# Performance work log

Hardware: AMD Instinct MI355X
Metric: run time of the kernel (lower is better)

Reference implementation:

```python
import jax, jax.numpy as jnp
import numpy as np

N_NODES = 100000
N_EDGES = 1600000
IN_CH = 256
OUT_CH = 64
BN_EPS = 1e-5


def gcn_conv(x, edge_index, W, b, n_nodes):
    # PyG GCNConv: h = x @ W; add self-loops; symmetric normalization; scatter-add at dst; + bias
    h = x @ W  # [N, out]
    loop = jnp.arange(n_nodes, dtype=edge_index.dtype)
    src = jnp.concatenate([edge_index[0], loop])
    dst = jnp.concatenate([edge_index[1], loop])
    deg = jnp.zeros((n_nodes,), h.dtype).at[dst].add(jnp.ones((), h.dtype))
    dinv = jnp.where(deg > 0, jax.lax.rsqrt(deg), 0.0)
    norm = dinv[src] * dinv[dst]  # [E+N]
    msg = h[src] * norm[:, None]  # gather + scale
    out = jax.ops.segment_sum(msg, dst, num_segments=n_nodes)
    return out + b


def batch_norm(x, gamma, beta):
    mu = x.mean(axis=0)
    var = x.var(axis=0)  # biased, as torch BN training stats
    return (x - mu) * jax.lax.rsqrt(var + BN_EPS) * gamma + beta


def setup_inputs() -> dict:
    key = jax.random.key(0)
    ks = jax.random.split(key, 8)
    x = jax.random.normal(ks[0], (N_NODES, IN_CH), dtype=jnp.float32)
    edge_index = jax.random.randint(ks[1], (2, N_EDGES), 0, N_NODES, dtype=jnp.int32)
    def glorot(k, fan_in, fan_out):
        s = (6.0 / (fan_in + fan_out)) ** 0.5
        return jax.random.uniform(k, (fan_in, fan_out), jnp.float32, -s, s)
    return {
        "x": x,
        "edge_index": edge_index,
        "W1": glorot(ks[2], IN_CH, 128), "b1": jnp.zeros((128,), jnp.float32),
        "gamma1": jnp.ones((128,), jnp.float32), "beta1": jnp.zeros((128,), jnp.float32),
        "W2": glorot(ks[3], 128, 64), "b2": jnp.zeros((64,), jnp.float32),
        "gamma2": jnp.ones((64,), jnp.float32), "beta2": jnp.zeros((64,), jnp.float32),
        "W3": glorot(ks[4], 64, OUT_CH), "b3": jnp.zeros((OUT_CH,), jnp.float32),
    }


def reference(x, edge_index, W1, b1, gamma1, beta1, W2, b2, gamma2, beta2, W3, b3):
    n = x.shape[0]
    h = gcn_conv(x, edge_index, W1, b1, n)
    h = jax.nn.relu(batch_norm(h, gamma1, beta1))  # dropout = identity (eval)
    h = gcn_conv(h, edge_index, W2, b2, n)
    h = jax.nn.relu(batch_norm(h, gamma2, beta2))
    z = gcn_conv(h, edge_index, W3, b3, n)
    return z
```

## Files before the change

### kernel.cpp

```cpp
#include <hip/hip_runtime.h>
#include <cstdint>
#include <cstddef>

#define IN_CH 256

constexpr float BN_EPS = 1e-5f;

using u16x4 = __attribute__((ext_vector_type(4))) unsigned short;
using u16x8 = __attribute__((ext_vector_type(8))) unsigned short;
using bf16x8 = __attribute__((ext_vector_type(8))) short;
using f32x4 = __attribute__((ext_vector_type(4))) float;

__device__ __forceinline__ unsigned short f2bf_rne(float x) {
  unsigned u = __builtin_bit_cast(unsigned, x);
  unsigned r = u + 0x7FFFu + ((u >> 16) & 1u);
  return (unsigned short)(r >> 16);
}
__device__ __forceinline__ float bf2f(unsigned short h) {
  unsigned u = ((unsigned)h) << 16;
  return __builtin_bit_cast(float, u);
}


#define NBK_MAX 400

__global__ __launch_bounds__(256) void bucket_hist(const int* __restrict__ dst,
                                                   int* __restrict__ bcnt, int E, int nbk) {
  __shared__ int c[NBK_MAX];
  for (int j = threadIdx.x; j < nbk; j += 256) c[j] = 0;
  __syncthreads();
  for (int i = blockIdx.x * 256 + threadIdx.x; i < E; i += gridDim.x * 256)
    atomicAdd(&c[dst[i] >> 8], 1);
  __syncthreads();
  for (int j = threadIdx.x; j < nbk; j += 256)
    if (c[j]) atomicAdd(&bcnt[j], c[j]);
}

__global__ void bucket_scan(const int* __restrict__ bcnt, int* __restrict__ boff,
                            int* __restrict__ gcur, int E, int nbk) {
  __shared__ int lds[512];
  int t = threadIdx.x;
  int v = (t < nbk) ? bcnt[t] : 0;
  lds[t] = v;
  __syncthreads();
  for (int s = 1; s < 512; s <<= 1) {
    int x = (t >= s) ? lds[t - s] : 0;
    __syncthreads();
    lds[t] += x;
    __syncthreads();
  }
  if (t < nbk) {
    boff[t] = lds[t] - v;
    gcur[t] = lds[t] - v;
  }
  if (t == 0) boff[nbk] = E;
}

__global__ __launch_bounds__(256) void partition(const int* __restrict__ src,
                                                 const int* __restrict__ dst,
                                                 int* __restrict__ gcur,
                                                 unsigned* __restrict__ part, int E, int nbk) {
  __shared__ int cnt[NBK_MAX];
  __shared__ int base[NBK_MAX];
  const int t = threadIdx.x;
  for (int j = t; j < nbk; j += 256) cnt[j] = 0;
  __syncthreads();
  const int e0 = blockIdx.x * 4096;
  unsigned mypk[16];
  int mybk[16];
#pragma unroll
  for (int u = 0; u < 16; ++u) {
    int e = e0 + u * 256 + t;
    if (e < E) {
      int d = dst[e];
      mypk[u] = (unsigned)src[e] | ((unsigned)(d & 255) << 17);
      mybk[u] = d >> 8;
      atomicAdd(&cnt[mybk[u]], 1);
    } else {
      mybk[u] = -1;
    }
  }
  __syncthreads();
  for (int j = t; j < nbk; j += 256) {
    int c = cnt[j];
    base[j] = c ? atomicAdd(&gcur[j], c) : 0;
    cnt[j] = 0;
  }
  __syncthreads();
#pragma unroll
  for (int u = 0; u < 16; ++u) {
    if (mybk[u] >= 0) {
      int r = atomicAdd(&cnt[mybk[u]], 1);
      part[base[mybk[u]] + r] = mypk[u];
    }
  }
}

__global__ __launch_bounds__(256) void bucket_csr(const unsigned* __restrict__ part,
                                                  const int* __restrict__ boff,
                                                  int* __restrict__ offs, int* __restrict__ srcs,
                                                  float* __restrict__ dinv, int N, int E) {
  __shared__ unsigned pk[8192];
  __shared__ int ssrc[8192];
  __shared__ int cnt[256];
  __shared__ int offl[256];
  __shared__ int cur[256];
  const int b = blockIdx.x;
  const int t = threadIdx.x;
  const int e0 = boff[b];
  int ne = boff[b + 1] - e0;
  if (ne > 8192) ne = 8192;
  cnt[t] = 0;
  __syncthreads();
  for (int i = t; i < ne; i += 256) {
    unsigned v = part[e0 + i];
    pk[i] = v;
    atomicAdd(&cnt[v >> 17], 1);
  }
  __syncthreads();
  int vv = cnt[t];
  offl[t] = vv;
  __syncthreads();
  for (int s = 1; s < 256; s <<= 1) {
    int x = (t >= s) ? offl[t - s] : 0;
    __syncthreads();
    offl[t] += x;
    __syncthreads();
  }
  int excl = offl[t] - vv;
  cur[t] = excl;
  __syncthreads();
  for (int i = t; i < ne; i += 256) {
    unsigned p = pk[i];
    int dl = p >> 17;
    int r = atomicAdd(&cur[dl], 1);
    ssrc[r] = (int)(p & 0x1FFFF);
  }
  __syncthreads();
  for (int i = t; i < ne; i += 256) srcs[e0 + i] = ssrc[i];
  int node = b * 256 + t;
  if (node < N) {
    offs[node] = e0 + excl;
    dinv[node] = rsqrtf((float)(vv + 1));
  }
  if (b == gridDim.x - 1 && t == 0) offs[N] = E;
}


__global__ void wprep(const float* __restrict__ W, unsigned short* __restrict__ hi,
                      unsigned short* __restrict__ lo, int K, int N) {
  int i = blockIdx.x * 256 + threadIdx.x;
  if (i >= K * N) return;
  int k = i / N, n = i - k * N;
  float v = W[i];
  unsigned short h = f2bf_rne(v);
  hi[(size_t)n * K + k] = h;
  lo[(size_t)n * K + k] = f2bf_rne(v - bf2f(h));
}


template <int K, int BN, int SLICES, bool BNRELU>
__global__ __launch_bounds__(256) void mfma_gemm(const float* __restrict__ A,
                                                 const unsigned short* __restrict__ Bt_hi,
                                                 const unsigned short* __restrict__ Bt_lo,
                                                 const float* __restrict__ ss,
                                                 const float* __restrict__ dinv,
                                                 unsigned short* __restrict__ Out, int M) {
  constexpr int BM = 128;
  constexpr int CS = BN / SLICES;
  __shared__ unsigned short Ah[BM * 32];
  __shared__ unsigned short Al[BM * 32];
  __shared__ unsigned short Bh[BN * 32];
  __shared__ unsigned short Bl[BN * 32];

  const int tid = threadIdx.x;
  const int wave = tid >> 6;
  const int lane = tid & 63;
  const int lg = lane >> 4;
  const int lr = lane & 15;
  const int row0 = blockIdx.x * BM;

  f32x4 acc[2][BN / 16];
#pragma unroll
  for (int f = 0; f < 2; ++f)
#pragma unroll
    for (int j = 0; j < BN / 16; ++j) acc[f][j] = (f32x4){0.f, 0.f, 0.f, 0.f};

  for (int k0 = 0; k0 < K; k0 += 32) {
    __syncthreads();
#pragma unroll
    for (int it = 0; it < 4; ++it) {
      int m = it * 32 + (tid >> 3);
      int c2 = tid & 7;
      float4 v = {0.f, 0.f, 0.f, 0.f};
      if (row0 + m < M) v = *(const float4*)&A[(size_t)(row0 + m) * K + k0 + c2 * 4];
      if constexpr (BNRELU) {
        int kk = k0 + c2 * 4;
        float4 sc = *(const float4*)&ss[kk];
        float4 sh = *(const float4*)&ss[K + kk];
        v.x = fmaxf(0.f, fmaf(v.x, sc.x, sh.x));
        v.y = fmaxf(0.f, fmaf(v.y, sc.y, sh.y));
        v.z = fmaxf(0.f, fmaf(v.z, sc.z, sh.z));
        v.w = fmaxf(0.f, fmaf(v.w, sc.w, sh.w));
      }
      float vv[4] = {v.x, v.y, v.z, v.w};
      u16x4 h4, l4;
#pragma unroll
      for (int i = 0; i < 4; ++i) {
        unsigned short h = f2bf_rne(vv[i]);
        h4[i] = h;
        l4[i] = f2bf_rne(vv[i] - bf2f(h));
      }
      int pr = (m >> 1) & 3;
      int base = m * 32 + (((c2 >> 1) ^ pr) * 8) + (c2 & 1) * 4;
      *(u16x4*)&Ah[base] = h4;
      *(u16x4*)&Al[base] = l4;
    }
#pragma unroll
    for (int it = 0; it < BN / 64; ++it) {
      int n = it * 64 + (tid >> 2);
      int c = tid & 3;
      int pr = (n >> 1) & 3;
      int base = n * 32 + ((c ^ pr) * 8);
      *(u16x8*)&Bh[base] = *(const u16x8*)&Bt_hi[(size_t)n * K + k0 + c * 8];
      *(u16x8*)&Bl[base] = *(const u16x8*)&Bt_lo[(size_t)n * K + k0 + c * 8];
    }
    __syncthreads();

    bf16x8 afh[2], afl[2];
#pragma unroll
    for (int f = 0; f < 2; ++f) {
      int m = wave * 32 + f * 16 + lr;
      int pr = (m >> 1) & 3;
      int base = m * 32 + ((lg ^ pr) * 8);
      afh[f] = *(const bf16x8*)&Ah[base];
      afl[f] = *(const bf16x8*)&Al[base];
    }
#pragma unroll
    for (int j = 0; j < BN / 16; ++j) {
      int n = j * 16 + lr;
      int pr = (n >> 1) & 3;
      int base = n * 32 + ((lg ^ pr) * 8);
      bf16x8 bh = *(const bf16x8*)&Bh[base];
      bf16x8 bl = *(const bf16x8*)&Bl[base];
#pragma unroll
      for (int f = 0; f < 2; ++f) {
        acc[f][j] = __builtin_amdgcn_mfma_f32_16x16x32_bf16(afh[f], bh, acc[f][j], 0, 0, 0);
        acc[f][j] = __builtin_amdgcn_mfma_f32_16x16x32_bf16(afl[f], bh, acc[f][j], 0, 0, 0);
        acc[f][j] = __builtin_amdgcn_mfma_f32_16x16x32_bf16(afh[f], bl, acc[f][j], 0, 0, 0);
      }
    }
  }

#pragma unroll
  for (int f = 0; f < 2; ++f) {
#pragma unroll
    for (int r4 = 0; r4 < 4; ++r4) {
      int r = row0 + wave * 32 + f * 16 + lg * 4 + r4;
      if (r >= M) continue;
      float dv = dinv[r];
#pragma unroll
      for (int j = 0; j < BN / 16; ++j) {
        int c = j * 16 + lr;
        int slice = c / CS;
        int wi = c % CS;
        Out[((size_t)slice * M + r) * CS + wi] = f2bf_rne(acc[f][j][r4] * dv);
      }
    }
  }
}


template <int C, int NSLICE, bool STATS, bool BIAS>
__global__ __launch_bounds__(256) void agg_slice(const unsigned short* __restrict__ g,
                                                 const int* __restrict__ offs,
                                                 const int* __restrict__ srcs,
                                                 const float* __restrict__ dinv,
                                                 const float* __restrict__ bias,
                                                 float* __restrict__ out,
                                                 float* __restrict__ stat, int N) {
  constexpr int CS = C / NSLICE;
  constexpr int LPE = CS / 2;
  constexpr int NPW = 64 / LPE;
  constexpr int T = 128 / (4 * NPW);
  const int s = blockIdx.x;
  const int w = threadIdx.x >> 6;
  const int lane = threadIdx.x & 63;
  const int gi = lane / LPE;
  const int ch2 = lane % LPE;
  const unsigned short* gs = g + (size_t)s * N * CS;
  const size_t cb = (size_t)ch2 * 2;

  float sx = 0.f, sy = 0.f, qx = 0.f, qy = 0.f;

#pragma unroll
  for (int it = 0; it < T; ++it) {
    int node = blockIdx.y * 128 + it * (4 * NPW) + w * NPW + gi;
    if (node < N) {
      unsigned u = *(const unsigned*)&gs[(size_t)node * CS + cb];
      float ax = __builtin_bit_cast(float, u << 16);
      float ay = __builtin_bit_cast(float, u & 0xffff0000u);

      const int e0 = offs[node], e1 = offs[node + 1];
      const int nb = (e1 - e0 + 7) >> 3;
      int sA[8], sB[8];
#pragma unroll
      for (int j = 0; j < 8; ++j) sA[j] = srcs[e0 + j];
      for (int b = 0; b < nb; ++b) {
        const int base = e0 + b * 8;
#pragma unroll
        for (int j = 0; j < 8; ++j) sB[j] = srcs[base + 8 + j];
        unsigned uu[8];
#pragma unroll
        for (int j = 0; j < 8; ++j) {
          uu[j] = 0u;
          if (base + j < e1) uu[j] = *(const unsigned*)&gs[(size_t)sA[j] * CS + cb];
        }
#pragma unroll
        for (int j = 0; j < 8; ++j) {
          ax += __builtin_bit_cast(float, uu[j] << 16);
          ay += __builtin_bit_cast(float, uu[j] & 0xffff0000u);
        }
#pragma unroll
        for (int j = 0; j < 8; ++j) sA[j] = sB[j];
      }
      float dv = dinv[node];
      float ox = ax * dv, oy = ay * dv;
      if constexpr (BIAS) {
        ox += bias[s * CS + cb];
        oy += bias[s * CS + cb + 1];
      }
      *(float2*)&out[(size_t)node * C + s * CS + cb] = (float2){ox, oy};
      if constexpr (STATS) {
        sx += ox;
        sy += oy;
        qx += ox * ox;
        qy += oy * oy;
      }
    }
  }

  if constexpr (STATS) {
    __shared__ float red[256][4];
    red[threadIdx.x][0] = sx;
    red[threadIdx.x][1] = sy;
    red[threadIdx.x][2] = qx;
    red[threadIdx.x][3] = qy;
    __syncthreads();
    if (threadIdx.x < LPE) {
      float a0 = 0.f, a1 = 0.f, a2 = 0.f, a3 = 0.f;
      for (int k = threadIdx.x; k < 256; k += LPE) {
        a0 += red[k][0];
        a1 += red[k][1];
        a2 += red[k][2];
        a3 += red[k][3];
      }
      atomicAdd(&stat[s * CS + threadIdx.x * 2], a0);
      atomicAdd(&stat[s * CS + threadIdx.x * 2 + 1], a1);
      atomicAdd(&stat[C + s * CS + threadIdx.x * 2], a2);
      atomicAdd(&stat[C + s * CS + threadIdx.x * 2 + 1], a3);
    }
  }
}


template <int C>
__global__ void bn_finalize(const float* __restrict__ stat, const float* __restrict__ gamma,
                            const float* __restrict__ beta, float* __restrict__ ss, int N) {
  int c = threadIdx.x;
  if (c >= C) return;
  float mu = stat[c] / (float)N;
  float var = stat[C + c] / (float)N - mu * mu;
  float rs = rsqrtf(var + BN_EPS);
  float sc = gamma[c] * rs;
  ss[c] = sc;
  ss[C + c] = beta[c] - mu * sc;
}


extern "C" void kernel_launch(void* const* d_in, const int* in_sizes, int n_in, void* d_out,
                              int out_size, void* d_ws, size_t ws_size, hipStream_t stream) {
  const float* x = (const float*)d_in[0];
  const int* ei = (const int*)d_in[1];
  const float* W1 = (const float*)d_in[2];
  const float* gamma1 = (const float*)d_in[4];
  const float* beta1 = (const float*)d_in[5];
  const float* W2 = (const float*)d_in[6];
  const float* gamma2 = (const float*)d_in[8];
  const float* beta2 = (const float*)d_in[9];
  const float* W3 = (const float*)d_in[10];
  const float* b3 = (const float*)d_in[11];
  float* out = (float*)d_out;

  const int N = in_sizes[0] / IN_CH;
  const int E = in_sizes[1] / 2;
  const int* e_src = ei;
  const int* e_dst = ei + E;
  const int nbk = (N + 255) >> 8;

  char* ws = (char*)d_ws;
  size_t off = 0;
  auto alloc = [&](size_t bytes) {
    size_t r = off;
    off += (bytes + 1023) & ~(size_t)1023;
    return r;
  };
  int* bcnt = (int*)(ws + alloc(NBK_MAX * 4));
  int* boff = (int*)(ws + alloc((NBK_MAX + 1) * 4));
  int* gcur = (int*)(ws + alloc(NBK_MAX * 4));
  unsigned* part = (unsigned*)(ws + alloc((size_t)E * 4));
  int* offs = (int*)(ws + alloc((size_t)(N + 1) * 4));
  int* srcs = (int*)(ws + alloc(((size_t)E + 32) * 4));
  float* dinv = (float*)(ws + alloc((size_t)N * 4));
  unsigned short* Wt1h = (unsigned short*)(ws + alloc(256 * 128 * 2));
  unsigned short* Wt1l = (unsigned short*)(ws + alloc(256 * 128 * 2));
  unsigned short* Wt2h = (unsigned short*)(ws + alloc(128 * 64 * 2));
  unsigned short* Wt2l = (unsigned short*)(ws + alloc(128 * 64 * 2));
  unsigned short* Wt3h = (unsigned short*)(ws + alloc(64 * 64 * 2));
  unsigned short* Wt3l = (unsigned short*)(ws + alloc(64 * 64 * 2));
  float* stat1 = (float*)(ws + alloc(256 * 4));
  float* stat2 = (float*)(ws + alloc(128 * 4));
  float* ss1 = (float*)(ws + alloc(256 * 4));
  float* ss2 = (float*)(ws + alloc(128 * 4));
  unsigned short* g = (unsigned short*)(ws + alloc((size_t)N * 128 * 2));
  float* h = (float*)(ws + alloc((size_t)N * 128 * 4));

  hipMemsetAsync(bcnt, 0, NBK_MAX * 4, stream);
  hipMemsetAsync(stat1, 0, 256 * 4, stream);
  hipMemsetAsync(stat2, 0, 128 * 4, stream);

  bucket_hist<<<2048, 256, 0, stream>>>(e_dst, bcnt, E, nbk);
  bucket_scan<<<1, 512, 0, stream>>>(bcnt, boff, gcur, E, nbk);
  partition<<<(E + 4095) / 4096, 256, 0, stream>>>(e_src, e_dst, gcur, part, E, nbk);
  bucket_csr<<<nbk, 256, 0, stream>>>(part, boff, offs, srcs, dinv, N, E);

  wprep<<<(256 * 128 + 255) / 256, 256, 0, stream>>>(W1, Wt1h, Wt1l, 256, 128);
  wprep<<<(128 * 64 + 255) / 256, 256, 0, stream>>>(W2, Wt2h, Wt2l, 128, 64);
  wprep<<<(64 * 64 + 255) / 256, 256, 0, stream>>>(W3, Wt3h, Wt3l, 64, 64);

  const int gM = (N + 127) / 128;
  const int nch = (N + 127) / 128;
  const dim3 gAgg1(8, nch);
  const dim3 gAgg2(4, nch);

  mfma_gemm<256, 128, 8, false><<<gM, 256, 0, stream>>>(x, Wt1h, Wt1l, nullptr, dinv, g, N);
  agg_slice<128, 8, true, false><<<gAgg1, 256, 0, stream>>>(g, offs, srcs, dinv, nullptr, h,
                                                            stat1, N);
  bn_finalize<128><<<1, 128, 0, stream>>>(stat1, gamma1, beta1, ss1, N);

  mfma_gemm<128, 64, 4, true><<<gM, 256, 0, stream>>>(h, Wt2h, Wt2l, ss1, dinv, g, N);
  agg_slice<64, 4, true, false><<<gAgg2, 256, 0, stream>>>(g, offs, srcs, dinv, nullptr, h,
                                                           stat2, N);
  bn_finalize<64><<<1, 64, 0, stream>>>(stat2, gamma2, beta2, ss2, N);

  mfma_gemm<64, 64, 4, true><<<gM, 256, 0, stream>>>(h, Wt3h, Wt3l, ss2, dinv, g, N);
  agg_slice<64, 4, false, true><<<gAgg2, 256, 0, stream>>>(g, offs, srcs, dinv, b3, out, nullptr,
                                                           N);
}
```

Measured before the change: 371.9 us.

## Store intermediate activations as bf16 and widen aggregation lanes to 4 channels

Intermediate aggregated features between layers are now written as bf16 instead of fp32, and the following GEMM reads bf16 directly. This halves the write and read traffic on the hidden buffer. The aggregation kernel now has each lane own 4 channels (8-byte gathers) rather than 2, with source indices pre-shifted into byte offsets to save address arithmetic. It also uses nontemporal loads and stores for the index stream and outputs. The risk is extra rounding in the intermediate activations, and fewer lanes per edge could change gather efficiency.

```diff
diff --git a/kernel.cpp b/kernel.cpp
--- a/kernel.cpp
+++ b/kernel.cpp
@@ -19,6 +19,12 @@
 __device__ __forceinline__ float bf2f(unsigned short h) {
   unsigned u = ((unsigned)h) << 16;
   return __builtin_bit_cast(float, u);
+}
+__device__ __forceinline__ float lo16f(unsigned u) {
+  return __builtin_bit_cast(float, u << 16);
+}
+__device__ __forceinline__ float hi16f(unsigned u) {
+  return __builtin_bit_cast(float, u & 0xffff0000u);
 }
 
 
@@ -134,7 +140,7 @@
     unsigned p = pk[i];
     int dl = p >> 17;
     int r = atomicAdd(&cur[dl], 1);
-    ssrc[r] = (int)(p & 0x1FFFF);
+    ssrc[r] = (int)(p & 0x1FFFF) << 5;
   }
   __syncthreads();
   for (int i = t; i < ne; i += 256) srcs[e0 + i] = ssrc[i];
@@ -159,8 +165,8 @@
 }
 
 
-template <int K, int BN, int SLICES, bool BNRELU>
-__global__ __launch_bounds__(256) void mfma_gemm(const float* __restrict__ A,
+template <int K, int BN, int SLICES, bool BNRELU, bool ABF16>
+__global__ __launch_bounds__(256) void mfma_gemm(const void* __restrict__ Av,
                                                  const unsigned short* __restrict__ Bt_hi,
                                                  const unsigned short* __restrict__ Bt_lo,
                                                  const float* __restrict__ ss,
@@ -192,18 +198,32 @@
     for (int it = 0; it < 4; ++it) {
       int m = it * 32 + (tid >> 3);
       int c2 = tid & 7;
-      float4 v = {0.f, 0.f, 0.f, 0.f};
-      if (row0 + m < M) v = *(const float4*)&A[(size_t)(row0 + m) * K + k0 + c2 * 4];
+      float vv[4] = {0.f, 0.f, 0.f, 0.f};
+      if constexpr (ABF16) {
+        if (row0 + m < M) {
+          u16x4 r = *(const u16x4*)&(
+              (const unsigned short*)Av)[(size_t)(row0 + m) * K + k0 + c2 * 4];
+#pragma unroll
+          for (int i = 0; i < 4; ++i) vv[i] = bf2f(r[i]);
+        }
+      } else {
+        if (row0 + m < M) {
+          float4 v = *(const float4*)&((const float*)Av)[(size_t)(row0 + m) * K + k0 + c2 * 4];
+          vv[0] = v.x;
+          vv[1] = v.y;
+          vv[2] = v.z;
+          vv[3] = v.w;
+        }
+      }
       if constexpr (BNRELU) {
         int kk = k0 + c2 * 4;
         float4 sc = *(const float4*)&ss[kk];
         float4 sh = *(const float4*)&ss[K + kk];
-        v.x = fmaxf(0.f, fmaf(v.x, sc.x, sh.x));
-        v.y = fmaxf(0.f, fmaf(v.y, sc.y, sh.y));
-        v.z = fmaxf(0.f, fmaf(v.z, sc.z, sh.z));
-        v.w = fmaxf(0.f, fmaf(v.w, sc.w, sh.w));
-      }
-      float vv[4] = {v.x, v.y, v.z, v.w};
+        vv[0] = fmaxf(0.f, fmaf(vv[0], sc.x, sh.x));
+        vv[1] = fmaxf(0.f, fmaf(vv[1], sc.y, sh.y));
+        vv[2] = fmaxf(0.f, fmaf(vv[2], sc.z, sh.z));
+        vv[3] = fmaxf(0.f, fmaf(vv[3], sc.w, sh.w));
+      }
       u16x4 h4, l4;
 #pragma unroll
       for (int i = 0; i < 4; ++i) {
@@ -271,94 +291,114 @@
 }
 
 
-template <int C, int NSLICE, bool STATS, bool BIAS>
+template <int C, int NSLICE, bool STATS, bool FINAL>
 __global__ __launch_bounds__(256) void agg_slice(const unsigned short* __restrict__ g,
                                                  const int* __restrict__ offs,
-                                                 const int* __restrict__ srcs,
+                                                 const int* __restrict__ srcsb,
                                                  const float* __restrict__ dinv,
                                                  const float* __restrict__ bias,
-                                                 float* __restrict__ out,
+                                                 void* __restrict__ outv,
                                                  float* __restrict__ stat, int N) {
   constexpr int CS = C / NSLICE;
-  constexpr int LPE = CS / 2;
+  constexpr int LPE = 4;
   constexpr int NPW = 64 / LPE;
-  constexpr int T = 128 / (4 * NPW);
+  constexpr int T = 2;
   const int s = blockIdx.x;
   const int w = threadIdx.x >> 6;
   const int lane = threadIdx.x & 63;
-  const int gi = lane / LPE;
-  const int ch2 = lane % LPE;
-  const unsigned short* gs = g + (size_t)s * N * CS;
-  const size_t cb = (size_t)ch2 * 2;
-
-  float sx = 0.f, sy = 0.f, qx = 0.f, qy = 0.f;
+  const int gi = lane >> 2;
+  const int ch2 = lane & 3;
+  const char* lane_base = (const char*)(g + (size_t)s * N * CS) + ch2 * 8;
+  const int cb = ch2 * 4;
+
+  float ssum[4] = {0.f, 0.f, 0.f, 0.f};
+  float sq[4] = {0.f, 0.f, 0.f, 0.f};
 
 #pragma unroll
   for (int it = 0; it < T; ++it) {
     int node = blockIdx.y * 128 + it * (4 * NPW) + w * NPW + gi;
     if (node < N) {
-      unsigned u = *(const unsigned*)&gs[(size_t)node * CS + cb];
-      float ax = __builtin_bit_cast(float, u << 16);
-      float ay = __builtin_bit_cast(float, u & 0xffff0000u);
+      uint2 u0 = *(const uint2*)(lane_base + (size_t)node * (CS * 2));
+      float a0 = lo16f(u0.x), a1 = hi16f(u0.x), a2 = lo16f(u0.y), a3 = hi16f(u0.y);
 
       const int e0 = offs[node], e1 = offs[node + 1];
       const int nb = (e1 - e0 + 7) >> 3;
       int sA[8], sB[8];
 #pragma unroll
-      for (int j = 0; j < 8; ++j) sA[j] = srcs[e0 + j];
+      for (int j = 0; j < 8; ++j) sA[j] = __builtin_nontemporal_load(&srcsb[e0 + j]);
       for (int b = 0; b < nb; ++b) {
         const int base = e0 + b * 8;
 #pragma unroll
-        for (int j = 0; j < 8; ++j) sB[j] = srcs[base + 8 + j];
-        unsigned uu[8];
+        for (int j = 0; j < 8; ++j) sB[j] = __builtin_nontemporal_load(&srcsb[base + 8 + j]);
+        uint2 uu[8];
 #pragma unroll
         for (int j = 0; j < 8; ++j) {
-          uu[j] = 0u;
-          if (base + j < e1) uu[j] = *(const unsigned*)&gs[(size_t)sA[j] * CS + cb];
+          uu[j].x = 0u;
+          uu[j].y = 0u;
+          if (base + j < e1) uu[j] = *(const uint2*)(lane_base + (size_t)(unsigned)sA[j]);
         }
 #pragma unroll
         for (int j = 0; j < 8; ++j) {
-          ax += __builtin_bit_cast(float, uu[j] << 16);
-          ay += __builtin_bit_cast(float, uu[j] & 0xffff0000u);
+          a0 += lo16f(uu[j].x);
+          a1 += hi16f(uu[j].x);
+          a2 += lo16f(uu[j].y);
+          a3 += hi16f(uu[j].y);
         }
 #pragma unroll
         for (int j = 0; j < 8; ++j) sA[j] = sB[j];
       }
       float dv = dinv[node];
-      float ox = ax * dv, oy = ay * dv;
-      if constexpr (BIAS) {
-        ox += bias[s * CS + cb];
-        oy += bias[s * CS + cb + 1];
-      }
-      *(float2*)&out[(size_t)node * C + s * CS + cb] = (float2){ox, oy};
+      float o0 = a0 * dv, o1 = a1 * dv, o2 = a2 * dv, o3 = a3 * dv;
+      if constexpr (FINAL) {
+        o0 += bias[s * CS + cb];
+        o1 += bias[s * CS + cb + 1];
+        o2 += bias[s * CS + cb + 2];
+        o3 += bias[s * CS + cb + 3];
+        f32x4 o = {o0, o1, o2, o3};
+        __builtin_nontemporal_store(
+            o, (f32x4*)&((float*)outv)[(size_t)node * C + s * CS + cb]);
+      } else {
+        u16x4 ob = {f2bf_rne(o0), f2bf_rne(o1), f2bf_rne(o2), f2bf_rne(o3)};
+        __builtin_nontemporal_store(
+            __builtin_bit_cast(unsigned long long, ob),
+            (unsigned long long*)&((unsigned short*)outv)[(size_t)node * C + s * CS + cb]);
+      }
       if constexpr (STATS) {
-        sx += ox;
-        sy += oy;
-        qx += ox * ox;
-        qy += oy * oy;
+        ssum[0] += o0;
+        ssum[1] += o1;
+        ssum[2] += o2;
+        ssum[3] += o3;
+        sq[0] += o0 * o0;
+        sq[1] += o1 * o1;
+        sq[2] += o2 * o2;
+        sq[3] += o3 * o3;
       }
     }
   }
 
   if constexpr (STATS) {
-    __shared__ float red[256][4];
-    red[threadIdx.x][0] = sx;
-    red[threadIdx.x][1] = sy;
-    red[threadIdx.x][2] = qx;
-    red[threadIdx.x][3] = qy;
-    __syncthreads();
-    if (threadIdx.x < LPE) {
-      float a0 = 0.f, a1 = 0.f, a2 = 0.f, a3 = 0.f;
-      for (int k = threadIdx.x; k < 256; k += LPE) {
-        a0 += red[k][0];
-        a1 += red[k][1];
-        a2 += red[k][2];
-        a3 += red[k][3];
-      }
-      atomicAdd(&stat[s * CS + threadIdx.x * 2], a0);
-      atomicAdd(&stat[s * CS + threadIdx.x * 2 + 1], a1);
-      atomicAdd(&stat[C + s * CS + threadIdx.x * 2], a2);
-      atomicAdd(&stat[C + s * CS + threadIdx.x * 2 + 1], a3);
+    __shared__ float red[256][8];
+    const int t = threadIdx.x;
+#pragma unroll
+    for (int m = 0; m < 4; ++m) {
+      red[t][m] = ssum[m];
+      red[t][4 + m] = sq[m];
+    }
+    __syncthreads();
+    if (t < LPE) {
+      float a[4] = {0.f, 0.f, 0.f, 0.f}, b[4] = {0.f, 0.f, 0.f, 0.f};
+      for (int k = t; k < 256; k += LPE) {
+#pragma unroll
+        for (int m = 0; m < 4; ++m) {
+          a[m] += red[k][m];
+          b[m] += red[k][4 + m];
+        }
+      }
+#pragma unroll
+      for (int m = 0; m < 4; ++m) {
+        atomicAdd(&stat[s * CS + t * 4 + m], a[m]);
+        atomicAdd(&stat[C + s * CS + t * 4 + m], b[m]);
+      }
     }
   }
 }
@@ -423,7 +463,7 @@
   float* ss1 = (float*)(ws + alloc(256 * 4));
   float* ss2 = (float*)(ws + alloc(128 * 4));
   unsigned short* g = (unsigned short*)(ws + alloc((size_t)N * 128 * 2));
-  float* h = (float*)(ws + alloc((size_t)N * 128 * 4));
+  unsigned short* hb = (unsigned short*)(ws + alloc((size_t)N * 128 * 2));
 
   hipMemsetAsync(bcnt, 0, NBK_MAX * 4, stream);
   hipMemsetAsync(stat1, 0, 256 * 4, stream);
@@ -443,17 +483,18 @@
   const dim3 gAgg1(8, nch);
   const dim3 gAgg2(4, nch);
 
-  mfma_gemm<256, 128, 8, false><<<gM, 256, 0, stream>>>(x, Wt1h, Wt1l, nullptr, dinv, g, N);
-  agg_slice<128, 8, true, false><<<gAgg1, 256, 0, stream>>>(g, offs, srcs, dinv, nullptr, h,
+  mfma_gemm<256, 128, 8, false, false><<<gM, 256, 0, stream>>>(x, Wt1h, Wt1l, nullptr, dinv, g,
+                                                               N);
+  agg_slice<128, 8, true, false><<<gAgg1, 256, 0, stream>>>(g, offs, srcs, dinv, nullptr, hb,
                                                             stat1, N);
   bn_finalize<128><<<1, 128, 0, stream>>>(stat1, gamma1, beta1, ss1, N);
 
-  mfma_gemm<128, 64, 4, true><<<gM, 256, 0, stream>>>(h, Wt2h, Wt2l, ss1, dinv, g, N);
-  agg_slice<64, 4, true, false><<<gAgg2, 256, 0, stream>>>(g, offs, srcs, dinv, nullptr, h,
+  mfma_gemm<128, 64, 4, true, true><<<gM, 256, 0, stream>>>(hb, Wt2h, Wt2l, ss1, dinv, g, N);
+  agg_slice<64, 4, true, false><<<gAgg2, 256, 0, stream>>>(g, offs, srcs, dinv, nullptr, hb,
                                                            stat2, N);
   bn_finalize<64><<<1, 64, 0, stream>>>(stat2, gamma2, beta2, ss2, N);
 
-  mfma_gemm<64, 64, 4, true><<<gM, 256, 0, stream>>>(h, Wt3h, Wt3l, ss2, dinv, g, N);
+  mfma_gemm<64, 64, 4, true, true><<<gM, 256, 0, stream>>>(hb, Wt3h, Wt3l, ss2, dinv, g, N);
   agg_slice<64, 4, false, true><<<gAgg2, 256, 0, stream>>>(g, offs, srcs, dinv, b3, out, nullptr,
                                                            N);
 }
```

Result: slower. 501.7 us (+34.9%).

## Store intermediate activations in bf16 and pre-scale source indices to byte offsets

Applied to the files above, without the earlier changes.

Intermediate aggregation outputs (h between layers) are written as packed bf16 instead of fp32, and the next GEMM reads bf16 inputs. This halves the write and read traffic for the inter-layer activations. CSR source indices are pre-shifted by 5 so the gather computes byte offsets without a multiply, which hard-codes a 32-byte slice width (CS=16). Storing BN inputs in bf16 loses precision relative to fp32 while statistics are still accumulated in fp32.

```diff
diff --git a/kernel.cpp b/kernel.cpp
--- a/kernel.cpp
+++ b/kernel.cpp
@@ -19,6 +19,12 @@
 __device__ __forceinline__ float bf2f(unsigned short h) {
   unsigned u = ((unsigned)h) << 16;
   return __builtin_bit_cast(float, u);
+}
+__device__ __forceinline__ float lo16f(unsigned u) {
+  return __builtin_bit_cast(float, u << 16);
+}
+__device__ __forceinline__ float hi16f(unsigned u) {
+  return __builtin_bit_cast(float, u & 0xffff0000u);
 }
 
 
@@ -134,7 +140,7 @@
     unsigned p = pk[i];
     int dl = p >> 17;
     int r = atomicAdd(&cur[dl], 1);
-    ssrc[r] = (int)(p & 0x1FFFF);
+    ssrc[r] = (int)(p & 0x1FFFF) << 5;
   }
   __syncthreads();
   for (int i = t; i < ne; i += 256) srcs[e0 + i] = ssrc[i];
@@ -159,8 +165,8 @@
 }
 
 
-template <int K, int BN, int SLICES, bool BNRELU>
-__global__ __launch_bounds__(256) void mfma_gemm(const float* __restrict__ A,
+template <int K, int BN, int SLICES, bool BNRELU, bool ABF16>
+__global__ __launch_bounds__(256) void mfma_gemm(const void* __restrict__ Av,
                                                  const unsigned short* __restrict__ Bt_hi,
                                                  const unsigned short* __restrict__ Bt_lo,
                                                  const float* __restrict__ ss,
@@ -192,18 +198,32 @@
     for (int it = 0; it < 4; ++it) {
       int m = it * 32 + (tid >> 3);
       int c2 = tid & 7;
-      float4 v = {0.f, 0.f, 0.f, 0.f};
-      if (row0 + m < M) v = *(const float4*)&A[(size_t)(row0 + m) * K + k0 + c2 * 4];
+      float vv[4] = {0.f, 0.f, 0.f, 0.f};
+      if constexpr (ABF16) {
+        if (row0 + m < M) {
+          u16x4 r = *(const u16x4*)&(
+              (const unsigned short*)Av)[(size_t)(row0 + m) * K + k0 + c2 * 4];
+#pragma unroll
+          for (int i = 0; i < 4; ++i) vv[i] = bf2f(r[i]);
+        }
+      } else {
+        if (row0 + m < M) {
+          float4 v = *(const float4*)&((const float*)Av)[(size_t)(row0 + m) * K + k0 + c2 * 4];
+          vv[0] = v.x;
+          vv[1] = v.y;
+          vv[2] = v.z;
+          vv[3] = v.w;
+        }
+      }
       if constexpr (BNRELU) {
         int kk = k0 + c2 * 4;
         float4 sc = *(const float4*)&ss[kk];
         float4 sh = *(const float4*)&ss[K + kk];
-        v.x = fmaxf(0.f, fmaf(v.x, sc.x, sh.x));
-        v.y = fmaxf(0.f, fmaf(v.y, sc.y, sh.y));
-        v.z = fmaxf(0.f, fmaf(v.z, sc.z, sh.z));
-        v.w = fmaxf(0.f, fmaf(v.w, sc.w, sh.w));
-      }
-      float vv[4] = {v.x, v.y, v.z, v.w};
+        vv[0] = fmaxf(0.f, fmaf(vv[0], sc.x, sh.x));
+        vv[1] = fmaxf(0.f, fmaf(vv[1], sc.y, sh.y));
+        vv[2] = fmaxf(0.f, fmaf(vv[2], sc.z, sh.z));
+        vv[3] = fmaxf(0.f, fmaf(vv[3], sc.w, sh.w));
+      }
       u16x4 h4, l4;
 #pragma unroll
       for (int i = 0; i < 4; ++i) {
@@ -271,25 +291,25 @@
 }
 
 
-template <int C, int NSLICE, bool STATS, bool BIAS>
+template <int C, int NSLICE, bool STATS, bool FINAL>
 __global__ __launch_bounds__(256) void agg_slice(const unsigned short* __restrict__ g,
                                                  const int* __restrict__ offs,
-                                                 const int* __restrict__ srcs,
+                                                 const int* __restrict__ srcsb,
                                                  const float* __restrict__ dinv,
                                                  const float* __restrict__ bias,
-                                                 float* __restrict__ out,
+                                                 void* __restrict__ outv,
                                                  float* __restrict__ stat, int N) {
   constexpr int CS = C / NSLICE;
-  constexpr int LPE = CS / 2;
+  constexpr int LPE = 8;
   constexpr int NPW = 64 / LPE;
-  constexpr int T = 128 / (4 * NPW);
+  constexpr int T = 4;
   const int s = blockIdx.x;
   const int w = threadIdx.x >> 6;
   const int lane = threadIdx.x & 63;
-  const int gi = lane / LPE;
-  const int ch2 = lane % LPE;
-  const unsigned short* gs = g + (size_t)s * N * CS;
-  const size_t cb = (size_t)ch2 * 2;
+  const int gi = lane >> 3;
+  const int ch2 = lane & 7;
+  const char* lane_base = (const char*)(g + (size_t)s * N * CS) + ch2 * 4;
+  const int cb = ch2 * 2;
 
   float sx = 0.f, sy = 0.f, qx = 0.f, qy = 0.f;
 
@@ -297,40 +317,43 @@
   for (int it = 0; it < T; ++it) {
     int node = blockIdx.y * 128 + it * (4 * NPW) + w * NPW + gi;
     if (node < N) {
-      unsigned u = *(const unsigned*)&gs[(size_t)node * CS + cb];
-      float ax = __builtin_bit_cast(float, u << 16);
-      float ay = __builtin_bit_cast(float, u & 0xffff0000u);
+      unsigned u = *(const unsigned*)(lane_base + (size_t)node * (CS * 2));
+      float ax = lo16f(u);
+      float ay = hi16f(u);
 
       const int e0 = offs[node], e1 = offs[node + 1];
       const int nb = (e1 - e0 + 7) >> 3;
       int sA[8], sB[8];
 #pragma unroll
-      for (int j = 0; j < 8; ++j) sA[j] = srcs[e0 + j];
+      for (int j = 0; j < 8; ++j) sA[j] = srcsb[e0 + j];
       for (int b = 0; b < nb; ++b) {
         const int base = e0 + b * 8;
 #pragma unroll
-        for (int j = 0; j < 8; ++j) sB[j] = srcs[base + 8 + j];
+        for (int j = 0; j < 8; ++j) sB[j] = srcsb[base + 8 + j];
         unsigned uu[8];
 #pragma unroll
         for (int j = 0; j < 8; ++j) {
           uu[j] = 0u;
-          if (base + j < e1) uu[j] = *(const unsigned*)&gs[(size_t)sA[j] * CS + cb];
+          if (base + j < e1) uu[j] = *(const unsigned*)(lane_base + (size_t)(unsigned)sA[j]);
         }
 #pragma unroll
         for (int j = 0; j < 8; ++j) {
-          ax += __builtin_bit_cast(float, uu[j] << 16);
-          ay += __builtin_bit_cast(float, uu[j] & 0xffff0000u);
+          ax += lo16f(uu[j]);
+          ay += hi16f(uu[j]);
         }
 #pragma unroll
         for (int j = 0; j < 8; ++j) sA[j] = sB[j];
       }
       float dv = dinv[node];
       float ox = ax * dv, oy = ay * dv;
-      if constexpr (BIAS) {
+      if constexpr (FINAL) {
         ox += bias[s * CS + cb];
         oy += bias[s * CS + cb + 1];
-      }
-      *(float2*)&out[(size_t)node * C + s * CS + cb] = (float2){ox, oy};
+        *(float2*)&((float*)outv)[(size_t)node * C + s * CS + cb] = (float2){ox, oy};
+      } else {
+        unsigned ob = (unsigned)f2bf_rne(ox) | ((unsigned)f2bf_rne(oy) << 16);
+        ((unsigned*)outv)[((size_t)node * C + s * CS + cb) >> 1] = ob;
+      }
       if constexpr (STATS) {
         sx += ox;
         sy += oy;
@@ -423,7 +446,7 @@
   float* ss1 = (float*)(ws + alloc(256 * 4));
   float* ss2 = (float*)(ws + alloc(128 * 4));
   unsigned short* g = (unsigned short*)(ws + alloc((size_t)N * 128 * 2));
-  float* h = (float*)(ws + alloc((size_t)N * 128 * 4));
+  unsigned short* hb = (unsigned short*)(ws + alloc((size_t)N * 128 * 2));
 
   hipMemsetAsync(bcnt, 0, NBK_MAX * 4, stream);
   hipMemsetAsync(stat1, 0, 256 * 4, stream);
@@ -443,17 +466,18 @@
   const dim3 gAgg1(8, nch);
   const dim3 gAgg2(4, nch);
 
-  mfma_gemm<256, 128, 8, false><<<gM, 256, 0, stream>>>(x, Wt1h, Wt1l, nullptr, dinv, g, N);
-  agg_slice<128, 8, true, false><<<gAgg1, 256, 0, stream>>>(g, offs, srcs, dinv, nullptr, h,
+  mfma_gemm<256, 128, 8, false, false><<<gM, 256, 0, stream>>>(x, Wt1h, Wt1l, nullptr, dinv, g,
+                                                               N);
+  agg_slice<128, 8, true, false><<<gAgg1, 256, 0, stream>>>(g, offs, srcs, dinv, nullptr, hb,
                                                             stat1, N);
   bn_finalize<128><<<1, 128, 0, stream>>>(stat1, gamma1, beta1, ss1, N);
 
-  mfma_gemm<128, 64, 4, true><<<gM, 256, 0, stream>>>(h, Wt2h, Wt2l, ss1, dinv, g, N);
-  agg_slice<64, 4, true, false><<<gAgg2, 256, 0, stream>>>(g, offs, srcs, dinv, nullptr, h,
+  mfma_gemm<128, 64, 4, true, true><<<gM, 256, 0, stream>>>(hb, Wt2h, Wt2l, ss1, dinv, g, N);
+  agg_slice<64, 4, true, false><<<gAgg2, 256, 0, stream>>>(g, offs, srcs, dinv, nullptr, hb,
                                                            stat2, N);
   bn_finalize<64><<<1, 64, 0, stream>>>(stat2, gamma2, beta2, ss2, N);
 
-  mfma_gemm<64, 64, 4, true><<<gM, 256, 0, stream>>>(h, Wt3h, Wt3l, ss2, dinv, g, N);
+  mfma_gemm<64, 64, 4, true, true><<<gM, 256, 0, stream>>>(hb, Wt3h, Wt3l, ss2, dinv, g, N);
   agg_slice<64, 4, false, true><<<gAgg2, 256, 0, stream>>>(g, offs, srcs, dinv, b3, out, nullptr,
                                                            N);
 }
```

After: 376.9 us, median of 2. About the same (+1.3%).
